# Optimization experiments

Measured on AMD Instinct MI355X. Metric: run time of the kernel, lower is better.

## Reference

```python
import jax, jax.numpy as jnp
import numpy as np

SEQ_LEN = 1024
D_MODEL = 512
K_FILT = 24
HEADS = 8
R = 512  # must equal d_model for the module's forward to type-check
NFFT = 2048  # nearest power of two >= 2*SEQ_LEN-1
LN_EPS = 1e-5


def _spectral_filters():
    # Hankel matrix Z[i,j] = 2 / ((i+j)^3 - (i+j)), i,j in 1..T
    e = np.arange(1, SEQ_LEN + 1, dtype=np.float64)
    ipj = e[:, None] + e[None, :]
    Z = 2.0 / (ipj ** 3 - ipj)
    sigma, phi = np.linalg.eigh(Z)
    sigma_k = np.clip(sigma[-K_FILT:], 1e-9, None)
    phi_k = phi[:, -K_FILT:] * sigma_k ** 0.25
    return phi_k.astype(np.float32)  # (T, K)


def setup_inputs() -> dict:
    key = jax.random.key(0)
    ks = jax.random.split(key, 12)
    s = 0.02
    B = 2

    def lin(k):
        kw, kb = jax.random.split(k)
        return (jax.random.normal(kw, (D_MODEL, D_MODEL), jnp.float32) * s,
                jax.random.normal(kb, (D_MODEL,), jnp.float32) * s)

    Wq, bq = lin(ks[0]); Wk, bk = lin(ks[1]); Wv, bv = lin(ks[2])
    Wg, bg = lin(ks[3]); Wo, bo = lin(ks[4])
    return {
        'x': jax.random.normal(ks[5], (B, SEQ_LEN, D_MODEL), jnp.float32),
        'stu_filters': jnp.asarray(_spectral_filters()),
        'M_inputs': jax.random.normal(ks[6], (D_MODEL, R), jnp.float32) * s,
        'M_filters': jax.random.normal(ks[7], (K_FILT, R), jnp.float32) * s,
        'Wq': Wq, 'bq': bq, 'Wk': Wk, 'bk': bk, 'Wv': Wv, 'bv': bv,
        'Wg': Wg, 'bg': bg, 'Wo': Wo, 'bo': bo,
        'ln_w': jnp.ones((R,), jnp.float32),
        'ln_b': jnp.zeros((R,), jnp.float32),
    }


def _stu_conv(u, v):
    # u: (B, T, r), v: (T, r). FFT-based causal conv with sign featurization.
    T = u.shape[1]
    sgn = jnp.where(jnp.arange(T) % 2 == 1, -1.0, 1.0)[None, :, None]  # (1,T,1)
    Vf = jnp.fft.rfft(v[None, :, :, None], n=NFFT, axis=1)  # (1,F,r,1)
    U = jnp.stack([u, u * sgn], axis=-1)  # (B,T,r,2)
    Uf = jnp.fft.rfft(U, n=NFFT, axis=1)  # (B,F,r,2)
    conv = jnp.fft.irfft(Vf * Uf, n=NFFT, axis=1)[:, :T]  # (B,T,r,2)
    return conv[..., 0], conv[..., 1] * sgn


def _layernorm(x, w, b):
    mu = jnp.mean(x, axis=-1, keepdims=True)
    var = jnp.mean((x - mu) ** 2, axis=-1, keepdims=True)
    return (x - mu) * jax.lax.rsqrt(var + LN_EPS) * w + b


def reference(x, stu_filters, M_inputs, M_filters, Wq, bq, Wk, bk, Wv, bv,
              Wg, bg, Wo, bo, ln_w, ln_b):
    B, T, d = x.shape
    hd = d // HEADS
    # STU features
    u_proj = x @ M_inputs                    # (B,T,r)
    phi_proj = stu_filters @ M_filters       # (T,r)
    sp, sm = _stu_conv(u_proj, phi_proj)
    x_tilde = _layernorm(sp + sm, ln_w, ln_b)  # (B,T,r==d)
    # gated linear attention with gelu features and causal cumsum state
    def proj(W, b):
        y = (x @ W.T + b).reshape(B, T, HEADS, hd).transpose(0, 2, 1, 3)
        return jax.nn.gelu(y, approximate=True)
    Q = proj(Wq, bq); K = proj(Wk, bk); V = proj(Wv, bv)
    Zt = jnp.einsum('bhtp,bhtn->bhtpn', V, K)   # (B,H,T,hd,hd)
    Hc = jnp.cumsum(Zt, axis=2)
    Y = jnp.einsum('bhtp,bhtpn->bhtn', Q, Hc)   # (B,H,T,hd)
    Y_attn = Y.transpose(0, 2, 1, 3).reshape(B, T, d)
    gate = jax.nn.sigmoid(x @ Wg.T + bg)
    comb = gate * Y_attn + (1.0 - gate) * x_tilde
    return comb @ Wo.T + bo
```

## Files before the change

### kernel.cpp

```cpp
#include <hip/hip_runtime.h>
#include <hip/hip_bf16.h>

#define T_SEQ 1024
#define D_MOD 512
#define NHEAD 8
#define HDIM  64
#define R_DIM 512
#define BATCH 2

typedef __attribute__((ext_vector_type(8))) __bf16 bf16x8;
typedef __attribute__((ext_vector_type(4))) __bf16 bf16x4;
typedef __attribute__((ext_vector_type(4))) float f32x4;

__device__ __forceinline__ float ldin(const void* p, size_t i, int bf) {
    if (bf) return __bfloat162float(((const __hip_bfloat16*)p)[i]);
    return ((const float*)p)[i];
}
__device__ __forceinline__ void stout(void* p, size_t i, int bf, float v) {
    if (bf) ((__hip_bfloat16*)p)[i] = __float2bfloat16(v);
    else    ((float*)p)[i] = v;
}

__device__ __forceinline__ float gelu_f(float x) {
    return 0.5f * x * (1.f + tanhf(0.7978845608028654f * (x + 0.044715f * x * x * x)));
}

__device__ __forceinline__ bf16x8 cvt8(float4 a, float4 b) {
    bf16x8 t;
    t[0]=(__bf16)a.x; t[1]=(__bf16)a.y; t[2]=(__bf16)a.z; t[3]=(__bf16)a.w;
    t[4]=(__bf16)b.x; t[5]=(__bf16)b.y; t[6]=(__bf16)b.z; t[7]=(__bf16)b.w;
    return t;
}

template<int BF>
__global__ __launch_bounds__(256) void mega_gemm(
    const void* __restrict__ x, const void* __restrict__ Mi,
    const void* __restrict__ stf, const void* __restrict__ Mf,
    const void* __restrict__ Wq, const void* __restrict__ bq,
    const void* __restrict__ Wk, const void* __restrict__ bk,
    const void* __restrict__ Wv, const void* __restrict__ bv,
    const void* __restrict__ Wg, const void* __restrict__ bg,
    __bf16* __restrict__ fu, __bf16* __restrict__ fphi,
    __bf16* __restrict__ fQ, __bf16* __restrict__ fKT,
    __bf16* __restrict__ fV, __bf16* __restrict__ fG)
{
    const int tid = threadIdx.x;
    const int job = blockIdx.z;
    if (job == 6) {
        float4* zp = (float4*)(fphi + 524288);
        const int bid = blockIdx.y * 8 + blockIdx.x;
        const float4 z4 = make_float4(0.f, 0.f, 0.f, 0.f);
        #pragma unroll
        for (int q = 0; q < 8; ++q)
            zp[(size_t)bid * 2048 + q * 256 + tid] = z4;
        return;
    }
    constexpr int bf = BF;
    const void* A = x; const void* Bw; const void* bias = nullptr;
    int Kd = 512, act = 0; bool trb = true;
    switch (job) {
        case 0: Bw = Mi; trb = false; break;
        case 1: Bw = Wq; bias = bq; act = 1; break;
        case 2: Bw = Wk; bias = bk; act = 1; break;
        case 3: Bw = Wv; bias = bv; act = 1; break;
        case 4: Bw = Wg; bias = bg; act = 2; break;
        default: A = stf; Bw = Mf; trb = false; Kd = 32; break;
    }
    const int M = (job == 5) ? 1024 : 2048;
    const int m0 = blockIdx.y * 64;
    if (m0 >= M) return;
    const int n0 = blockIdx.x * 64;

    __shared__ __align__(16) __bf16 As[64][40];
    __shared__ __align__(16) __bf16 Bs[64][40];
    const int wave = tid >> 6, lane = tid & 63;
    const int lm = lane & 15, kq = lane >> 4;

    f32x4 acc[4] = {};

    for (int k0 = 0; k0 < Kd; k0 += 32) {
        if (k0) __syncthreads();
        {
            const int mo = tid >> 2;
            const int ko = (tid & 3) * 8;
            if (job == 5) {
                bf16x8 t;
                #pragma unroll
                for (int q = 0; q < 8; ++q) {
                    const int k = ko + q;
                    t[q] = (k < 24) ? (__bf16)ldin(A, (size_t)(m0 + mo) * 24 + k, bf)
                                    : (__bf16)0.f;
                }
                *(bf16x8*)&As[mo][ko] = t;
            } else if (bf) {
                *(bf16x8*)&As[mo][ko] =
                    *(const bf16x8*)((const __bf16*)A + (size_t)(m0 + mo) * 512 + k0 + ko);
            } else {
                const float* Af = (const float*)A + (size_t)(m0 + mo) * 512 + k0 + ko;
                *(bf16x8*)&As[mo][ko] = cvt8(*(const float4*)Af, *(const float4*)(Af + 4));
            }
        }
        if (trb) {
            const int no = tid >> 2;
            const int ko = (tid & 3) * 8;
            const int cs = ((((ko >> 3) ^ (no >> 3)) & 3) << 3);
            const size_t go = (size_t)(n0 + no) * 512 + k0 + ko;
            if (bf) {
                *(bf16x8*)&Bs[no][cs] = *(const bf16x8*)((const __bf16*)Bw + go);
            } else {
                const float* Bf = (const float*)Bw + go;
                *(bf16x8*)&Bs[no][cs] = cvt8(*(const float4*)Bf, *(const float4*)(Bf + 4));
            }
        } else {
            const int kk = tid >> 3;
            const int nn = (tid & 7) * 8;
            if (job == 5) {
                #pragma unroll
                for (int q = 0; q < 8; ++q) {
                    const int row = nn + q;
                    const int c = ((((kk >> 3) ^ (row >> 3)) & 3) << 3) | (kk & 7);
                    Bs[row][c] = (kk < 24) ? (__bf16)ldin(Bw, (size_t)kk * 512 + n0 + row, bf)
                                           : (__bf16)0.f;
                }
            } else {
                const size_t off = (size_t)(k0 + kk) * 512 + n0 + nn;
                bf16x8 t;
                if (bf) {
                    t = *(const bf16x8*)((const __bf16*)Bw + off);
                } else {
                    const float* Bf = (const float*)Bw + off;
                    t = cvt8(*(const float4*)Bf, *(const float4*)(Bf + 4));
                }
                #pragma unroll
                for (int q = 0; q < 8; ++q) {
                    const int row = nn + q;
                    const int c = ((((kk >> 3) ^ (row >> 3)) & 3) << 3) | (kk & 7);
                    Bs[row][c] = t[q];
                }
            }
        }
        __syncthreads();
        const bf16x8 a = *(const bf16x8*)&As[wave * 16 + lm][kq * 8];
        #pragma unroll
        for (int nt = 0; nt < 4; ++nt) {
            const int row = nt * 16 + lm;
            const bf16x8 b = *(const bf16x8*)&Bs[row][(((kq ^ (row >> 3)) & 3) << 3)];
            acc[nt] = __builtin_amdgcn_mfma_f32_16x16x32_bf16(a, b, acc[nt], 0, 0, 0);
        }
    }
    #pragma unroll
    for (int nt = 0; nt < 4; ++nt) {
        const int n = n0 + nt * 16 + lm;
        #pragma unroll
        for (int r2 = 0; r2 < 4; ++r2) {
            const int m = m0 + wave * 16 + kq * 4 + r2;
            float v = acc[nt][r2];
            if (bias) v += ldin(bias, (size_t)n, bf);
            if (act == 1) v = gelu_f(v);
            if (act == 2) v = 1.f / (1.f + expf(-v));
            switch (job) {
                case 0: fu[(size_t)m * 512 + n] = (__bf16)v; break;
                case 5: fphi[(size_t)m * 512 + n] = (__bf16)v; break;
                case 1: fQ[(size_t)m * 512 + n] = (__bf16)v; break;
                case 3: fV[(size_t)m * 512 + n] = (__bf16)v; break;
                case 4: fG[(size_t)m * 512 + n] = (__bf16)v; break;
                case 2: {
                    const int b = m >> 10, t = m & 1023;
                    const int h = n >> 6,  p = n & 63;
                    fKT[(((size_t)b * NHEAD + h) * 64 + p) * T_SEQ + t] = (__bf16)v;
                    break;
                }
            }
        }
    }
}

__global__ __launch_bounds__(256) void conv_attn_k(
    const __bf16* __restrict__ u, const __bf16* __restrict__ vphi,
    float* __restrict__ w,
    const __bf16* __restrict__ Q, const __bf16* __restrict__ KT,
    const __bf16* __restrict__ V, float* __restrict__ Y)
{
    __shared__ __align__(16) unsigned char smem[49152];
    const int tid = threadIdx.x;
    const int z = blockIdx.z;
    int rem = blockIdx.x, ti = 0;
    while (rem >= ((ti + 4) >> 2)) { rem -= (ti + 4) >> 2; ++ti; }
    const int jlo = rem * 4;
    const int jhi = (jlo + 3 < ti) ? jlo + 3 : ti;
    const int t0 = ti * 64;

    if (z < 2) {
        float (*vs)[64] = (float (*)[64])smem;
        float (*us)[64] = (float (*)[64])(smem + 16384);
        const int rl = tid & 63, tg = tid >> 6;
        const int b = z;
        const int r0 = blockIdx.y * 64;
        const __bf16* ub = u + (size_t)b * T_SEQ * R_DIM;
        float acc[16] = {};
        for (int j = jlo; j <= jhi; ++j) {
            if (j != jlo) __syncthreads();
            const int L0 = j * 64;
            const int W0 = t0 - L0 - 63;
            #pragma unroll
            for (int jj = 0; jj < 8; ++jj) {
                const int n = jj * 256 + tid;
                const int row = n >> 4, c4 = (n & 15) * 4;
                int s = W0 + row;
                s = s < 0 ? 0 : (s > T_SEQ - 1 ? T_SEQ - 1 : s);
                const bf16x4 t = *(const bf16x4*)&ub[(size_t)s * R_DIM + r0 + c4];
                *(float4*)&us[row][c4] =
                    make_float4((float)t[0], (float)t[1], (float)t[2], (float)t[3]);
            }
            #pragma unroll
            for (int jj = 0; jj < 4; ++jj) {
                const int n = jj * 256 + tid;
                const int row = n >> 4, c4 = (n & 15) * 4;
                const bf16x4 t = *(const bf16x4*)&vphi[(size_t)(L0 + row) * R_DIM + r0 + c4];
                *(float4*)&vs[row][c4] =
                    make_float4((float)t[0], (float)t[1], (float)t[2], (float)t[3]);
            }
            __syncthreads();
            if (j < ti) {
                #pragma unroll
                for (int g = 0; g < 4; ++g) {
                    const int wsmin = tg * 16 + 49 - 16 * g;
                    float ur[30];
                    #pragma unroll
                    for (int q = 0; q < 30; ++q) ur[q] = us[wsmin + q][rl];
                    float vr[8];
                    #pragma unroll
                    for (int e = 0; e < 8; ++e) vr[e] = vs[16 * g + 2 * e][rl];
                    #pragma unroll
                    for (int e = 0; e < 8; ++e)
                        #pragma unroll
                        for (int i = 0; i < 16; ++i)
                            acc[i] += vr[e] * ur[i - 2 * e + 14];
                }
            } else {
                for (int l = 0; l < 64; l += 2) {
                    const float vv = vs[l][rl];
                    #pragma unroll
                    for (int i = 0; i < 16; ++i) {
                        const int srel = tg * 16 + i - l;
                        if (srel >= 0) acc[i] += vv * us[srel + 63][rl];
                    }
                }
            }
        }
        #pragma unroll
        for (int i = 0; i < 16; ++i)
            atomicAdd(&w[((size_t)b * T_SEQ + t0 + tg * 16 + i) * R_DIM + r0 + rl],
                      2.f * acc[i]);
    } else {
        __bf16 (*Qs)[72] = (__bf16 (*)[72])smem;
        __bf16 (*Vs)[72] = (__bf16 (*)[72])(smem + 9216);
        __bf16 (*Kt)[72] = (__bf16 (*)[72])(smem + 18432);
        __bf16 (*Sa)[72] = (__bf16 (*)[72])(smem + 27648);
        const int wave = tid >> 6, lane = tid & 63;
        const int lm = lane & 15, kq = lane >> 4;
        const int b = z - 2;
        const int h = blockIdx.y;
        const size_t cbase = ((size_t)b * T_SEQ) * D_MOD + h * HDIM;
        const __bf16* KTh = KT + (((size_t)b * NHEAD + h) * 64) * T_SEQ;
        #pragma unroll
        for (int it = 0; it < 2; ++it) {
            const int n = it * 256 + tid;
            const int row = n >> 3, p0 = (n & 7) * 8;
            *(bf16x8*)&Qs[row][p0] = *(const bf16x8*)&Q[cbase + (size_t)(t0 + row) * D_MOD + p0];
        }
        f32x4 accY[4] = {};
        for (int j = jlo; j <= jhi; ++j) {
            const int s0 = j * 64;
            __syncthreads();
            #pragma unroll
            for (int it = 0; it < 2; ++it) {
                const int n = it * 256 + tid;
                const int row = n >> 3, c0 = (n & 7) * 8;
                *(bf16x8*)&Vs[row][c0] = *(const bf16x8*)&V[cbase + (size_t)(s0 + row) * D_MOD + c0];
                *(bf16x8*)&Kt[row][c0] = *(const bf16x8*)&KTh[(size_t)row * T_SEQ + s0 + c0];
            }
            __syncthreads();
            f32x4 sacc[4] = {};
            #pragma unroll
            for (int ks = 0; ks < 2; ++ks) {
                const bf16x8 a = *(const bf16x8*)&Qs[wave * 16 + lm][ks * 32 + kq * 8];
                #pragma unroll
                for (int nt = 0; nt < 4; ++nt) {
                    const bf16x8 bb = *(const bf16x8*)&Vs[nt * 16 + lm][ks * 32 + kq * 8];
                    sacc[nt] = __builtin_amdgcn_mfma_f32_16x16x32_bf16(a, bb, sacc[nt], 0, 0, 0);
                }
            }
            const bool diag = (j == ti);
            #pragma unroll
            for (int nt = 0; nt < 4; ++nt) {
                const int sl = nt * 16 + lm;
                #pragma unroll
                for (int r2 = 0; r2 < 4; ++r2) {
                    const int tl = wave * 16 + kq * 4 + r2;
                    float v = sacc[nt][r2];
                    if (diag && sl > tl) v = 0.f;
                    Sa[tl][sl] = (__bf16)v;
                }
            }
            #pragma unroll
            for (int ks = 0; ks < 2; ++ks) {
                const bf16x8 a = *(const bf16x8*)&Sa[wave * 16 + lm][ks * 32 + kq * 8];
                #pragma unroll
                for (int nt = 0; nt < 4; ++nt) {
                    const bf16x8 bb = *(const bf16x8*)&Kt[nt * 16 + lm][ks * 32 + kq * 8];
                    accY[nt] = __builtin_amdgcn_mfma_f32_16x16x32_bf16(a, bb, accY[nt], 0, 0, 0);
                }
            }
        }
        #pragma unroll
        for (int nt = 0; nt < 4; ++nt) {
            const int nh = nt * 16 + lm;
            #pragma unroll
            for (int r2 = 0; r2 < 4; ++r2) {
                const int tl = wave * 16 + kq * 4 + r2;
                atomicAdd(&Y[cbase + (size_t)(t0 + tl) * D_MOD + nh], accY[nt][r2]);
            }
        }
    }
}

__global__ __launch_bounds__(256) void stats_k(const float* __restrict__ w,
                                               float* __restrict__ stats)
{
    const int tid = threadIdx.x;
    const int r = tid >> 4, c = tid & 15;
    const int row = blockIdx.x * 16 + r;
    const float* p = w + (size_t)row * R_DIM;
    float s = 0.f, ss = 0.f;
    #pragma unroll
    for (int q = 0; q < 8; ++q) {
        const float4 v = *(const float4*)(p + c * 4 + q * 64);
        s  += v.x + v.y + v.z + v.w;
        ss += v.x * v.x + v.y * v.y + v.z * v.z + v.w * v.w;
    }
    s  += __shfl_xor(s, 1, 64);  s  += __shfl_xor(s, 2, 64);
    s  += __shfl_xor(s, 4, 64);  s  += __shfl_xor(s, 8, 64);
    ss += __shfl_xor(ss, 1, 64); ss += __shfl_xor(ss, 2, 64);
    ss += __shfl_xor(ss, 4, 64); ss += __shfl_xor(ss, 8, 64);
    if (c == 0) {
        const float mu = s * (1.f / 512.f);
        float var = ss * (1.f / 512.f) - mu * mu;
        var = var < 0.f ? 0.f : var;
        stats[row * 2]     = mu;
        stats[row * 2 + 1] = rsqrtf(var + 1e-5f);
    }
}

template<int BF>
__global__ __launch_bounds__(256) void final_gemm(const __bf16* __restrict__ G,
                                                  const float* __restrict__ Yf,
                                                  const float* __restrict__ Wf,
                                                  const float* __restrict__ stats,
                                                  const void* __restrict__ lnw,
                                                  const void* __restrict__ lnb,
                                                  const void* __restrict__ Wo,
                                                  const void* __restrict__ bo,
                                                  void* __restrict__ out)
{
    constexpr int bf = BF;
    __shared__ __align__(16) __bf16 sm[2][2 * 64 * 40];
    const int tid = threadIdx.x;
    const int wave = tid >> 6, lane = tid & 63;
    const int lm = lane & 15, kq = lane >> 4;
    const int mo = tid >> 2, ko = (tid & 3) * 8;
    const int m0 = blockIdx.y * 64, n0 = blockIdx.x * 64;

    const float2 st = *(const float2*)(stats + (size_t)(m0 + mo) * 2);
    const float mu = st.x, rs = st.y;

    bf16x8 pg, pw, pLg, pLb;
    float4 py0, py1, pv0, pv1, pw0, pw1, pLg0, pLg1, pLb0, pLb1;

    auto issue = [&](int k0) {
        const size_t off = (size_t)(m0 + mo) * 512 + k0 + ko;
        pg  = *(const bf16x8*)(G + off);
        py0 = *(const float4*)(Yf + off); py1 = *(const float4*)(Yf + off + 4);
        pv0 = *(const float4*)(Wf + off); pv1 = *(const float4*)(Wf + off + 4);
        const size_t ob = (size_t)(n0 + mo) * 512 + k0 + ko;
        if (bf) {
            pw  = *(const bf16x8*)((const __bf16*)Wo + ob);
            pLg = *(const bf16x8*)((const __bf16*)lnw + k0 + ko);
            pLb = *(const bf16x8*)((const __bf16*)lnb + k0 + ko);
        } else {
            const float* Bf = (const float*)Wo + ob;
            pw0 = *(const float4*)Bf; pw1 = *(const float4*)(Bf + 4);
            const float* Lg = (const float*)lnw + k0 + ko;
            pLg0 = *(const float4*)Lg; pLg1 = *(const float4*)(Lg + 4);
            const float* Lb = (const float*)lnb + k0 + ko;
            pLb0 = *(const float4*)Lb; pLb1 = *(const float4*)(Lb + 4);
        }
    };
    auto commit = [&](int bi) {
        __bf16 (*As)[40] = (__bf16 (*)[40])sm[bi];
        __bf16 (*Bs)[40] = (__bf16 (*)[40])(sm[bi] + 64 * 40);
        const float yv[8] = {py0.x,py0.y,py0.z,py0.w,py1.x,py1.y,py1.z,py1.w};
        const float wv[8] = {pv0.x,pv0.y,pv0.z,pv0.w,pv1.x,pv1.y,pv1.z,pv1.w};
        float gw[8], gb[8];
        if (bf) {
            #pragma unroll
            for (int q = 0; q < 8; ++q) { gw[q] = (float)pLg[q]; gb[q] = (float)pLb[q]; }
        } else {
            gw[0]=pLg0.x; gw[1]=pLg0.y; gw[2]=pLg0.z; gw[3]=pLg0.w;
            gw[4]=pLg1.x; gw[5]=pLg1.y; gw[6]=pLg1.z; gw[7]=pLg1.w;
            gb[0]=pLb0.x; gb[1]=pLb0.y; gb[2]=pLb0.z; gb[3]=pLb0.w;
            gb[4]=pLb1.x; gb[5]=pLb1.y; gb[6]=pLb1.z; gb[7]=pLb1.w;
        }
        bf16x8 t;
        #pragma unroll
        for (int q = 0; q < 8; ++q) {
            const float xt = (wv[q] - mu) * rs * gw[q] + gb[q];
            const float gg = (float)pg[q];
            t[q] = (__bf16)(gg * yv[q] + (1.f - gg) * xt);
        }
        *(bf16x8*)&As[mo][ko] = t;
        *(bf16x8*)&Bs[mo][ko] = bf ? pw : cvt8(pw0, pw1);
    };

    f32x4 acc[4] = {};
    issue(0);
    commit(0);
    __syncthreads();
    int cur = 0;
    for (int k0 = 0; k0 < 512; k0 += 32) {
        const bool haveNext = (k0 + 32 < 512);
        if (haveNext) issue(k0 + 32);
        __bf16 (*As)[40] = (__bf16 (*)[40])sm[cur];
        __bf16 (*Bs)[40] = (__bf16 (*)[40])(sm[cur] + 64 * 40);
        const bf16x8 a = *(const bf16x8*)&As[wave * 16 + lm][kq * 8];
        #pragma unroll
        for (int nt = 0; nt < 4; ++nt) {
            const bf16x8 b = *(const bf16x8*)&Bs[nt * 16 + lm][kq * 8];
            acc[nt] = __builtin_amdgcn_mfma_f32_16x16x32_bf16(a, b, acc[nt], 0, 0, 0);
        }
        if (haveNext) {
            commit(cur ^ 1);
            __syncthreads();
            cur ^= 1;
        }
    }
    #pragma unroll
    for (int nt = 0; nt < 4; ++nt) {
        const int n = n0 + nt * 16 + lm;
        #pragma unroll
        for (int r2 = 0; r2 < 4; ++r2) {
            const int m = m0 + wave * 16 + kq * 4 + r2;
            float v = acc[nt][r2] + ldin(bo, (size_t)n, bf);
            stout(out, (size_t)m * 512 + n, bf, v);
        }
    }
}

extern "C" void kernel_launch(void* const* d_in, const int* in_sizes, int n_in,
                              void* d_out, int out_size, void* d_ws, size_t ws_size,
                              hipStream_t stream)
{
    const void* x   = d_in[0];
    const void* stf = d_in[1];
    const void* Mi  = d_in[2];
    const void* Mf  = d_in[3];
    const void* Wq  = d_in[4];  const void* bq = d_in[5];
    const void* Wk  = d_in[6];  const void* bk = d_in[7];
    const void* Wv  = d_in[8];  const void* bv = d_in[9];
    const void* Wg  = d_in[10]; const void* bg = d_in[11];
    const void* Wo  = d_in[12]; const void* bo = d_in[13];
    const void* lnw = d_in[14]; const void* lnb = d_in[15];

    float* base = (float*)d_ws;
    __bf16* f_u   = (__bf16*)base;
    __bf16* f_phi = f_u + 1048576;
    float*  f_w   = base + 786432;
    float*  f_Y   = base + 1835008;
    __bf16* f_Q   = (__bf16*)(base + 3407872);
    __bf16* f_KT  = f_Q + 1048576;
    __bf16* f_V   = f_KT + 1048576;
    __bf16* f_G   = f_V + 1048576;
    float*  f_st  = (float*)(f_G + 1048576);

    const int bf = (in_sizes[0] == BATCH * T_SEQ * D_MOD * 2);

    dim3 blk(256);

    if (bf)
        mega_gemm<1><<<dim3(8, 32, 7), blk, 0, stream>>>(
            x, Mi, stf, Mf, Wq, bq, Wk, bk, Wv, bv, Wg, bg,
            f_u, f_phi, f_Q, f_KT, f_V, f_G);
    else
        mega_gemm<0><<<dim3(8, 32, 7), blk, 0, stream>>>(
            x, Mi, stf, Mf, Wq, bq, Wk, bk, Wv, bv, Wg, bg,
            f_u, f_phi, f_Q, f_KT, f_V, f_G);

    conv_attn_k<<<dim3(40, 8, 4), blk, 0, stream>>>(f_u, f_phi, f_w, f_Q, f_KT, f_V, f_Y);

    stats_k<<<dim3(128), blk, 0, stream>>>(f_w, f_st);

    if (bf) final_gemm<1><<<dim3(8, 32), blk, 0, stream>>>(f_G, f_Y, f_w, f_st, lnw, lnb, Wo, bo, d_out);
    else    final_gemm<0><<<dim3(8, 32), blk, 0, stream>>>(f_G, f_Y, f_w, f_st, lnw, lnb, Wo, bo, d_out);
}
```

Before: 164.8 us.

## Fuse Q/K/V/G projections into one block sharing the x tile

Restructures the first GEMM kernel so one block computes the Q, K, V and gate projections together. Each x tile is loaded into shared memory once and reused across four weight tiles, where before four separate job slices each reloaded it. The grid shrinks from 7 to 3 z-slices, and the zero-fill and phi jobs are folded into the third slice. In exchange each block holds 64 accumulator vectors and a 4x larger B buffer, so it uses more registers and LDS and fewer blocks run in parallel (256 fused blocks instead of 1024).

Result: slower. 170.4 us (+3.4%).

```diff
diff --git a/kernel.cpp b/kernel.cpp
--- a/kernel.cpp
+++ b/kernel.cpp
@@ -44,132 +44,167 @@
     __bf16* __restrict__ fQ, __bf16* __restrict__ fKT,
     __bf16* __restrict__ fV, __bf16* __restrict__ fG)
 {
+    constexpr int bf = BF;
     const int tid = threadIdx.x;
-    const int job = blockIdx.z;
-    if (job == 6) {
-        float4* zp = (float4*)(fphi + 524288);
-        const int bid = blockIdx.y * 8 + blockIdx.x;
-        const float4 z4 = make_float4(0.f, 0.f, 0.f, 0.f);
-        #pragma unroll
-        for (int q = 0; q < 8; ++q)
-            zp[(size_t)bid * 2048 + q * 256 + tid] = z4;
-        return;
-    }
-    constexpr int bf = BF;
-    const void* A = x; const void* Bw; const void* bias = nullptr;
-    int Kd = 512, act = 0; bool trb = true;
-    switch (job) {
-        case 0: Bw = Mi; trb = false; break;
-        case 1: Bw = Wq; bias = bq; act = 1; break;
-        case 2: Bw = Wk; bias = bk; act = 1; break;
-        case 3: Bw = Wv; bias = bv; act = 1; break;
-        case 4: Bw = Wg; bias = bg; act = 2; break;
-        default: A = stf; Bw = Mf; trb = false; Kd = 32; break;
-    }
-    const int M = (job == 5) ? 1024 : 2048;
+    const int z = blockIdx.z;
     const int m0 = blockIdx.y * 64;
-    if (m0 >= M) return;
     const int n0 = blockIdx.x * 64;
 
     __shared__ __align__(16) __bf16 As[64][40];
-    __shared__ __align__(16) __bf16 Bs[64][40];
+    __shared__ __align__(16) __bf16 Bs[4][64][40];
     const int wave = tid >> 6, lane = tid & 63;
     const int lm = lane & 15, kq = lane >> 4;
-
-    f32x4 acc[4] = {};
-
-    for (int k0 = 0; k0 < Kd; k0 += 32) {
-        if (k0) __syncthreads();
-        {
-            const int mo = tid >> 2;
-            const int ko = (tid & 3) * 8;
-            if (job == 5) {
+    const int mo = tid >> 2, ko = (tid & 3) * 8;
+
+    if (z == 0) {
+        const void* Wb[4] = {Wq, Wk, Wv, Wg};
+        const void* biases[4] = {bq, bk, bv, bg};
+        f32x4 acc[4][4] = {};
+        const int cs = ((((ko >> 3) ^ (mo >> 3)) & 3) << 3);
+
+        for (int k0 = 0; k0 < 512; k0 += 32) {
+            if (k0) __syncthreads();
+            if (bf) {
+                *(bf16x8*)&As[mo][ko] =
+                    *(const bf16x8*)((const __bf16*)x + (size_t)(m0 + mo) * 512 + k0 + ko);
+            } else {
+                const float* Af = (const float*)x + (size_t)(m0 + mo) * 512 + k0 + ko;
+                *(bf16x8*)&As[mo][ko] = cvt8(*(const float4*)Af, *(const float4*)(Af + 4));
+            }
+            const size_t go = (size_t)(n0 + mo) * 512 + k0 + ko;
+            #pragma unroll
+            for (int jb = 0; jb < 4; ++jb) {
+                if (bf) {
+                    *(bf16x8*)&Bs[jb][mo][cs] =
+                        *(const bf16x8*)((const __bf16*)Wb[jb] + go);
+                } else {
+                    const float* Bf = (const float*)Wb[jb] + go;
+                    *(bf16x8*)&Bs[jb][mo][cs] = cvt8(*(const float4*)Bf, *(const float4*)(Bf + 4));
+                }
+            }
+            __syncthreads();
+            const bf16x8 a = *(const bf16x8*)&As[wave * 16 + lm][kq * 8];
+            #pragma unroll
+            for (int jb = 0; jb < 4; ++jb) {
+                #pragma unroll
+                for (int nt = 0; nt < 4; ++nt) {
+                    const int row = nt * 16 + lm;
+                    const bf16x8 b = *(const bf16x8*)&Bs[jb][row][(((kq ^ (row >> 3)) & 3) << 3)];
+                    acc[jb][nt] = __builtin_amdgcn_mfma_f32_16x16x32_bf16(a, b, acc[jb][nt], 0, 0, 0);
+                }
+            }
+        }
+        #pragma unroll
+        for (int jb = 0; jb < 4; ++jb) {
+            #pragma unroll
+            for (int nt = 0; nt < 4; ++nt) {
+                const int n = n0 + nt * 16 + lm;
+                #pragma unroll
+                for (int r2 = 0; r2 < 4; ++r2) {
+                    const int m = m0 + wave * 16 + kq * 4 + r2;
+                    float v = acc[jb][nt][r2] + ldin(biases[jb], (size_t)n, bf);
+                    v = (jb == 3) ? 1.f / (1.f + expf(-v)) : gelu_f(v);
+                    if (jb == 0)      fQ[(size_t)m * 512 + n] = (__bf16)v;
+                    else if (jb == 2) fV[(size_t)m * 512 + n] = (__bf16)v;
+                    else if (jb == 3) fG[(size_t)m * 512 + n] = (__bf16)v;
+                    else {
+                        const int b = m >> 10, t = m & 1023;
+                        const int h = n >> 6,  p = n & 63;
+                        fKT[(((size_t)b * NHEAD + h) * 64 + p) * T_SEQ + t] = (__bf16)v;
+                    }
+                }
+            }
+        }
+    } else if (z == 1) {
+        f32x4 acc[4] = {};
+        const int kk = tid >> 3, nn = (tid & 7) * 8;
+        for (int k0 = 0; k0 < 512; k0 += 32) {
+            if (k0) __syncthreads();
+            if (bf) {
+                *(bf16x8*)&As[mo][ko] =
+                    *(const bf16x8*)((const __bf16*)x + (size_t)(m0 + mo) * 512 + k0 + ko);
+            } else {
+                const float* Af = (const float*)x + (size_t)(m0 + mo) * 512 + k0 + ko;
+                *(bf16x8*)&As[mo][ko] = cvt8(*(const float4*)Af, *(const float4*)(Af + 4));
+            }
+            {
+                const size_t off = (size_t)(k0 + kk) * 512 + n0 + nn;
                 bf16x8 t;
-                #pragma unroll
-                for (int q = 0; q < 8; ++q) {
-                    const int k = ko + q;
-                    t[q] = (k < 24) ? (__bf16)ldin(A, (size_t)(m0 + mo) * 24 + k, bf)
-                                    : (__bf16)0.f;
-                }
-                *(bf16x8*)&As[mo][ko] = t;
-            } else if (bf) {
-                *(bf16x8*)&As[mo][ko] =
-                    *(const bf16x8*)((const __bf16*)A + (size_t)(m0 + mo) * 512 + k0 + ko);
-            } else {
-                const float* Af = (const float*)A + (size_t)(m0 + mo) * 512 + k0 + ko;
-                *(bf16x8*)&As[mo][ko] = cvt8(*(const float4*)Af, *(const float4*)(Af + 4));
-            }
-        }
-        if (trb) {
-            const int no = tid >> 2;
-            const int ko = (tid & 3) * 8;
-            const int cs = ((((ko >> 3) ^ (no >> 3)) & 3) << 3);
-            const size_t go = (size_t)(n0 + no) * 512 + k0 + ko;
-            if (bf) {
-                *(bf16x8*)&Bs[no][cs] = *(const bf16x8*)((const __bf16*)Bw + go);
-            } else {
-                const float* Bf = (const float*)Bw + go;
-                *(bf16x8*)&Bs[no][cs] = cvt8(*(const float4*)Bf, *(const float4*)(Bf + 4));
-            }
-        } else {
-            const int kk = tid >> 3;
-            const int nn = (tid & 7) * 8;
-            if (job == 5) {
+                if (bf) {
+                    t = *(const bf16x8*)((const __bf16*)Mi + off);
+                } else {
+                    const float* Bf = (const float*)Mi + off;
+                    t = cvt8(*(const float4*)Bf, *(const float4*)(Bf + 4));
+                }
                 #pragma unroll
                 for (int q = 0; q < 8; ++q) {
                     const int row = nn + q;
                     const int c = ((((kk >> 3) ^ (row >> 3)) & 3) << 3) | (kk & 7);
-                    Bs[row][c] = (kk < 24) ? (__bf16)ldin(Bw, (size_t)kk * 512 + n0 + row, bf)
-                                           : (__bf16)0.f;
-                }
-            } else {
-                const size_t off = (size_t)(k0 + kk) * 512 + n0 + nn;
-                bf16x8 t;
-                if (bf) {
-                    t = *(const bf16x8*)((const __bf16*)Bw + off);
-                } else {
-                    const float* Bf = (const float*)Bw + off;
-                    t = cvt8(*(const float4*)Bf, *(const float4*)(Bf + 4));
-                }
-                #pragma unroll
-                for (int q = 0; q < 8; ++q) {
-                    const int row = nn + q;
-                    const int c = ((((kk >> 3) ^ (row >> 3)) & 3) << 3) | (kk & 7);
-                    Bs[row][c] = t[q];
-                }
-            }
+                    Bs[0][row][c] = t[q];
+                }
+            }
+            __syncthreads();
+            const bf16x8 a = *(const bf16x8*)&As[wave * 16 + lm][kq * 8];
+            #pragma unroll
+            for (int nt = 0; nt < 4; ++nt) {
+                const int row = nt * 16 + lm;
+                const bf16x8 b = *(const bf16x8*)&Bs[0][row][(((kq ^ (row >> 3)) & 3) << 3)];
+                acc[nt] = __builtin_amdgcn_mfma_f32_16x16x32_bf16(a, b, acc[nt], 0, 0, 0);
+            }
+        }
+        #pragma unroll
+        for (int nt = 0; nt < 4; ++nt) {
+            const int n = n0 + nt * 16 + lm;
+            #pragma unroll
+            for (int r2 = 0; r2 < 4; ++r2) {
+                const int m = m0 + wave * 16 + kq * 4 + r2;
+                fu[(size_t)m * 512 + n] = (__bf16)acc[nt][r2];
+            }
+        }
+    } else {
+        if (blockIdx.y >= 16) {
+            float4* zp = (float4*)(fphi + 524288);
+            const int bid = (blockIdx.y - 16) * 8 + blockIdx.x;
+            const float4 z4 = make_float4(0.f, 0.f, 0.f, 0.f);
+            #pragma unroll
+            for (int q = 0; q < 16; ++q)
+                zp[(size_t)bid * 4096 + q * 256 + tid] = z4;
+            return;
+        }
+        f32x4 acc[4] = {};
+        const int kk = tid >> 3, nn = (tid & 7) * 8;
+        {
+            bf16x8 t;
+            #pragma unroll
+            for (int q = 0; q < 8; ++q) {
+                const int k = ko + q;
+                t[q] = (k < 24) ? (__bf16)ldin(stf, (size_t)(m0 + mo) * 24 + k, bf)
+                                : (__bf16)0.f;
+            }
+            *(bf16x8*)&As[mo][ko] = t;
+        }
+        #pragma unroll
+        for (int q = 0; q < 8; ++q) {
+            const int row = nn + q;
+            const int c = ((((kk >> 3) ^ (row >> 3)) & 3) << 3) | (kk & 7);
+            Bs[0][row][c] = (kk < 24) ? (__bf16)ldin(Mf, (size_t)kk * 512 + n0 + row, bf)
+                                      : (__bf16)0.f;
         }
         __syncthreads();
         const bf16x8 a = *(const bf16x8*)&As[wave * 16 + lm][kq * 8];
         #pragma unroll
         for (int nt = 0; nt < 4; ++nt) {
             const int row = nt * 16 + lm;
-            const bf16x8 b = *(const bf16x8*)&Bs[row][(((kq ^ (row >> 3)) & 3) << 3)];
+            const bf16x8 b = *(const bf16x8*)&Bs[0][row][(((kq ^ (row >> 3)) & 3) << 3)];
             acc[nt] = __builtin_amdgcn_mfma_f32_16x16x32_bf16(a, b, acc[nt], 0, 0, 0);
         }
-    }
-    #pragma unroll
-    for (int nt = 0; nt < 4; ++nt) {
-        const int n = n0 + nt * 16 + lm;
-        #pragma unroll
-        for (int r2 = 0; r2 < 4; ++r2) {
-            const int m = m0 + wave * 16 + kq * 4 + r2;
-            float v = acc[nt][r2];
-            if (bias) v += ldin(bias, (size_t)n, bf);
-            if (act == 1) v = gelu_f(v);
-            if (act == 2) v = 1.f / (1.f + expf(-v));
-            switch (job) {
-                case 0: fu[(size_t)m * 512 + n] = (__bf16)v; break;
-                case 5: fphi[(size_t)m * 512 + n] = (__bf16)v; break;
-                case 1: fQ[(size_t)m * 512 + n] = (__bf16)v; break;
-                case 3: fV[(size_t)m * 512 + n] = (__bf16)v; break;
-                case 4: fG[(size_t)m * 512 + n] = (__bf16)v; break;
-                case 2: {
-                    const int b = m >> 10, t = m & 1023;
-                    const int h = n >> 6,  p = n & 63;
-                    fKT[(((size_t)b * NHEAD + h) * 64 + p) * T_SEQ + t] = (__bf16)v;
-                    break;
-                }
+        #pragma unroll
+        for (int nt = 0; nt < 4; ++nt) {
+            const int n = n0 + nt * 16 + lm;
+            #pragma unroll
+            for (int r2 = 0; r2 < 4; ++r2) {
+                const int m = m0 + wave * 16 + kq * 4 + r2;
+                fphi[(size_t)m * 512 + n] = (__bf16)acc[nt][r2];
             }
         }
     }
@@ -487,11 +522,11 @@
     dim3 blk(256);
 
     if (bf)
-        mega_gemm<1><<<dim3(8, 32, 7), blk, 0, stream>>>(
+        mega_gemm<1><<<dim3(8, 32, 3), blk, 0, stream>>>(
             x, Mi, stf, Mf, Wq, bq, Wk, bk, Wv, bv, Wg, bg,
             f_u, f_phi, f_Q, f_KT, f_V, f_G);
     else
-        mega_gemm<0><<<dim3(8, 32, 7), blk, 0, stream>>>(
+        mega_gemm<0><<<dim3(8, 32, 3), blk, 0, stream>>>(
             x, Mi, stf, Mf, Wq, bq, Wk, bk, Wv, bv, Wg, bg,
             f_u, f_phi, f_Q, f_KT, f_V, f_G);
 
```
